# Kernel optimization log

Hardware: AMD Instinct MI355X
Metric: run time of the kernel (lower is better)

The kernel has to match this reference:

```python
import jax, jax.numpy as jnp
import numpy as np
from jax import lax

B, W, M = 4, 20, 512
RNN_HID = 64
N_HIDDEN = RNN_HID          # bi = False
HALF = N_HIDDEN // 2
K = 10
LONG_K = W // 2             # conv_long kernel
LONG_OUT = W - 2 * (LONG_K - 1)   # = 2
N_SPATIAL = 10


def setup_inputs() -> dict:
    key = jax.random.key(0)
    ks = jax.random.split(key, 24)
    g = lambda i, shape, s=0.05: jax.random.normal(ks[i], shape, jnp.float32) * s
    return {
        "x": jax.random.normal(ks[0], (B, W, M), jnp.float32),
        # vanilla RNN (tanh), 1 layer, input_size=1
        "W_ih": g(1, (RNN_HID, 1), 0.2), "W_hh": g(2, (RNN_HID, RNN_HID), 0.1),
        "b_ih": g(3, (RNN_HID,)), "b_hh": g(4, (RNN_HID,)),
        # attention adjacency params
        "W1": g(5, (HALF, N_HIDDEN), 0.1), "b1": g(6, (HALF,)),
        "W2": g(7, (HALF, N_HIDDEN), 0.1),
        "V": g(8, (HALF,), 0.1), "bv": g(9, (1,)),
        "Wb": g(10, (M, M), 0.05), "wb": g(11, (1,)),
        # conv / conv_long
        "conv_w": g(12, (K, 1, W), 0.1), "conv_b": g(13, (K,)),
        "convl_w": g(14, (K, 1, LONG_K), 0.1), "convl_b": g(15, (K,)),
        # graph conv layers: adj @ (x @ W) + b
        "gc1_w": g(16, ((1 + LONG_OUT) * K, N_HIDDEN), 0.1), "gc1_b": g(17, (N_HIDDEN,)),
        "gc2_w": g(18, (N_HIDDEN, N_SPATIAL), 0.1), "gc2_b": g(19, (N_SPATIAL,)),
        # output head
        "out_w": g(20, (1, N_HIDDEN + N_SPATIAL), 0.1), "out_b": g(21, (1,)),
        # fixed geographic adjacency (data.adj)
        "adj": jax.random.uniform(ks[22], (M, M), dtype=jnp.float32),
    }


def _conv1d(x, w, b, dilation=1):
    # x: (N, Cin, W), w: (Cout, Cin, K) -> (N, Cout, Wout), VALID padding
    y = lax.conv_general_dilated(x, w, (1,), 'VALID', rhs_dilation=(dilation,),
                                 dimension_numbers=('NCH', 'OIH', 'NCH'))
    return y + b[None, :, None]


def reference(x, W_ih, W_hh, b_ih, b_hh, W1, b1, W2, V, bv, Wb, wb,
              conv_w, conv_b, convl_w, convl_b, gc1_w, gc1_b, gc2_w, gc2_b,
              out_w, out_b, adj):
    b, w, m = x.shape
    # ---- RNN encode each node's scalar series: (b*m, w, 1) -> last hidden ----
    xr = jnp.transpose(x, (0, 2, 1)).reshape(b * m, w)          # (bm, w)
    inp = xr[..., None] @ W_ih.T + b_ih                         # (bm, w, H)

    def step(h, u):
        return jnp.tanh(u + h @ W_hh.T + b_hh), None

    h0 = jnp.zeros((b * m, RNN_HID), x.dtype)
    h_last, _ = lax.scan(step, h0, jnp.swapaxes(inp, 0, 1))     # (bm, H)
    last_hid = h_last.reshape(b, m, N_HIDDEN)
    out_temporal = last_hid

    # ---- pairwise bilinear attention adjacency (broadcast instead of repeat) ----
    p = last_hid @ W1.T                                         # (b, m, H/2)
    q = last_hid @ W2.T                                         # (b, m, H/2)
    e = jax.nn.elu(p[:, :, None, :] + q[:, None, :, :] + b1)    # (b, m, m, H/2)
    a_mx = e @ V + bv[0]                                        # (b, m, m)
    # F.normalize(p=2, dim=1)
    nrm = jnp.maximum(jnp.sqrt(jnp.sum(a_mx * a_mx, axis=1, keepdims=True)), 1e-12)
    a_mx = a_mx / nrm
    c = jax.nn.sigmoid(a_mx @ Wb + wb[0])                       # (b, m, m)
    A = adj[None] * c + a_mx * (1.0 - c)

    # ---- per-node convs, batched over all b*m series (no Python loop) ----
    h_tmp = xr[:, None, :]                                      # (bm, 1, w)
    r = _conv1d(h_tmp, conv_w, conv_b)                          # (bm, k, 1)
    r_long = _conv1d(h_tmp, convl_w, convl_b, dilation=2)       # (bm, k, long_out)
    r_l = jnp.concatenate([r, r_long], axis=-1).reshape(b, m, -1)  # (b, m, (1+lo)*k)
    r_l = jax.nn.relu(r_l)

    # ---- graph convolutions: adj @ (x @ W) + b ----
    xg = jax.nn.relu(A @ (r_l @ gc1_w) + gc1_b)                 # (b, m, H)
    out_spatial = jax.nn.relu(A @ (xg @ gc2_w) + gc2_b)         # (b, m, 10)

    out = jnp.concatenate([out_spatial, out_temporal], axis=-1)
    return (out @ out_w.T + out_b)[..., 0]                      # (b, m)
```

## Files before the change

kernel.cpp:

```cpp
#include <hip/hip_runtime.h>
#include <hip/hip_bf16.h>
#include <cstdint>
#include <cstddef>

#define OFF_P     0
#define OFF_QB    65536
#define OFF_TDOT  131072
#define OFF_COLSQ 133120
#define OFF_ZT    135168
#define OFF_AMXB  155648
#define OFF_ABF   679936
#define OFF_G1T   1204224
#define OFF_WBT   1269760

typedef __attribute__((ext_vector_type(8))) short short8;
typedef __attribute__((ext_vector_type(8))) unsigned short ushort8;
typedef __attribute__((ext_vector_type(4))) float f32x4;

__device__ inline unsigned short f2bf(float f) {
    unsigned u = __builtin_bit_cast(unsigned, f);
    unsigned r = u + 0x7FFFu + ((u >> 16) & 1u);
    return (unsigned short)(r >> 16);
}
__device__ inline float bf2f(unsigned short s) {
    unsigned u = ((unsigned)s) << 16;
    return __builtin_bit_cast(float, u);
}
__device__ inline float tanh_fast(float x) {
    return 1.f - 2.f/(__expf(2.f*x) + 1.f);
}

__global__ __launch_bounds__(256) void k1_rnn(
    const float* __restrict__ x, const float* __restrict__ W_ih,
    const float* __restrict__ W_hh, const float* __restrict__ b_ih,
    const float* __restrict__ b_hh, const float* __restrict__ W1,
    const float* __restrict__ b1, const float* __restrict__ W2,
    const float* __restrict__ conv_w, const float* __restrict__ conv_b,
    const float* __restrict__ convl_w, const float* __restrict__ convl_b,
    const float* __restrict__ gc1_w, const float* __restrict__ out_w,
    const float* __restrict__ out_b, const float* __restrict__ Wb,
    float* __restrict__ p_out, float* __restrict__ qb_out,
    unsigned short* __restrict__ G1T, float* __restrict__ tdot,
    float* __restrict__ colsq, unsigned short* __restrict__ WbT)
{
    __shared__ float h_sh[4][64];
    __shared__ float xt_sh[4][20];
    __shared__ float rl_sh[4][30];
    __shared__ float tile[64][68];
    int tid = threadIdx.x;

    if (blockIdx.x >= 512) {
        int tt = blockIdx.x - 512;
        int k0 = (tt >> 3) * 64, j0 = (tt & 7) * 64;
        #pragma unroll
        for (int q = 0; q < 4; ++q) {
            int kr = (tid>>4) + 16*q;
            int jc = (tid&15)*4;
            *(float4*)&tile[kr][jc] = *(const float4*)(Wb + (size_t)(k0+kr)*512 + j0 + jc);
        }
        __syncthreads();
        int jl = tid>>2, kc = (tid&3)*16;
        int j = j0 + jl;
        ushort8 v0, v1;
        #pragma unroll
        for (int kk = 0; kk < 8; ++kk) v0[kk] = f2bf(tile[kc+kk][jl]);
        #pragma unroll
        for (int kk = 0; kk < 8; ++kk) v1[kk] = f2bf(tile[kc+8+kk][jl]);
        unsigned short* dst = WbT + (size_t)j*512 + k0 + kc;
        *(ushort8*)dst = v0;
        *(ushort8*)(dst+8) = v1;
        return;
    }

    int w = tid >> 6, lane = tid & 63;
    int s = blockIdx.x * 4 + w;
    int b = s >> 9, m = s & 511;

    if (blockIdx.x < 8) colsq[blockIdx.x * 256 + tid] = 0.f;

    if (lane < 20) xt_sh[w][lane] = x[(b*20 + lane)*512 + m];

    float wrow[64];
    const float* wr = W_hh + lane*64;
    #pragma unroll
    for (int k4 = 0; k4 < 16; ++k4) {
        float4 v = reinterpret_cast<const float4*>(wr)[k4];
        wrow[4*k4+0]=v.x; wrow[4*k4+1]=v.y; wrow[4*k4+2]=v.z; wrow[4*k4+3]=v.w;
    }
    float wih = W_ih[lane], bih = b_ih[lane], bhh = b_hh[lane];
    h_sh[w][lane] = 0.f;
    float h = 0.f;

    if (lane < 10) {
        float acc = conv_b[lane];
        #pragma unroll
        for (int t = 0; t < 20; ++t) acc += conv_w[lane*20+t]*xt_sh[w][t];
        rl_sh[w][3*lane] = fmaxf(acc, 0.f);
    } else if (lane < 30) {
        int idx = lane-10, j = idx>>1, oo = idx&1;
        float acc = convl_b[j];
        #pragma unroll
        for (int t = 0; t < 10; ++t) acc += convl_w[j*10+t]*xt_sh[w][oo+2*t];
        rl_sh[w][3*j+1+oo] = fmaxf(acc, 0.f);
    }

    for (int t = 0; t < 20; ++t) {
        float a0=0.f, a1=0.f, a2=0.f, a3=0.f;
        #pragma unroll
        for (int k = 0; k < 64; k += 4) {
            a0 += wrow[k+0]*h_sh[w][k+0];
            a1 += wrow[k+1]*h_sh[w][k+1];
            a2 += wrow[k+2]*h_sh[w][k+2];
            a3 += wrow[k+3]*h_sh[w][k+3];
        }
        float acc = xt_sh[w][t]*wih + bih + bhh + ((a0+a1)+(a2+a3));
        h = tanh_fast(acc);
        h_sh[w][lane] = h;
    }

    float td = h * out_w[10 + lane];
    #pragma unroll
    for (int off = 32; off; off >>= 1) td += __shfl_down(td, off);
    if (lane == 0) tdot[s] = td + out_b[0];

    if (lane < 32) {
        const float* w1r = W1 + lane*64;
        float acc = 0.f;
        #pragma unroll
        for (int k = 0; k < 64; ++k) acc += w1r[k]*h_sh[w][k];
        p_out[s*32 + lane] = acc;
    } else {
        int i = lane - 32;
        const float* w2r = W2 + i*64;
        float acc = 0.f;
        #pragma unroll
        for (int k = 0; k < 64; ++k) acc += w2r[k]*h_sh[w][k];
        qb_out[s*32 + i] = acc + b1[i];
    }

    float g = 0.f;
    #pragma unroll
    for (int t = 0; t < 30; ++t) g += rl_sh[w][t]*gc1_w[t*64 + lane];
    G1T[((size_t)(b*64 + lane))*512 + m] = f2bf(g);
}

__global__ __launch_bounds__(256) void k2_amx(
    const float* __restrict__ p, const float* __restrict__ qb,
    const float* __restrict__ V, const float* __restrict__ bv,
    unsigned short* __restrict__ amxB, float* __restrict__ colsq)
{
    __shared__ float p_sh[32*36], q_sh[32*36], v_sh[32], sq_sh[32*17];
    int t = threadIdx.x;
    int b = blockIdx.z, i0 = blockIdx.y*32, j0 = blockIdx.x*32;
    {
        int r = t >> 3, c4 = (t & 7)*4;
        *(float4*)&p_sh[r*36 + c4] = *(const float4*)(p  + (size_t)(b*512 + i0 + r)*32 + c4);
        *(float4*)&q_sh[r*36 + c4] = *(const float4*)(qb + (size_t)(b*512 + j0 + r)*32 + c4);
    }
    if (t < 32) v_sh[t] = V[t];
    __syncthreads();

    int ti = t >> 4, tj = t & 15;
    float bv0 = bv[0];
    float a00 = bv0, a01 = bv0, a10 = bv0, a11 = bv0;
    #pragma unroll
    for (int h = 0; h < 32; ++h) {
        float p0 = p_sh[ti*36 + h], p1 = p_sh[(ti+16)*36 + h];
        float q0 = q_sh[tj*36 + h], q1 = q_sh[(tj+16)*36 + h];
        float vh = v_sh[h];
        float x00 = p0+q0, x01 = p0+q1, x10 = p1+q0, x11 = p1+q1;
        float e00 = x00 > 0.f ? x00 : __expf(x00)-1.f;
        float e01 = x01 > 0.f ? x01 : __expf(x01)-1.f;
        float e10 = x10 > 0.f ? x10 : __expf(x10)-1.f;
        float e11 = x11 > 0.f ? x11 : __expf(x11)-1.f;
        a00 += vh*e00; a01 += vh*e01; a10 += vh*e10; a11 += vh*e11;
    }
    size_t base0 = ((size_t)(b*512 + i0 + ti))*512 + j0;
    size_t base1 = ((size_t)(b*512 + i0 + ti + 16))*512 + j0;
    amxB[base0 + tj]      = f2bf(a00);
    amxB[base0 + tj + 16] = f2bf(a01);
    amxB[base1 + tj]      = f2bf(a10);
    amxB[base1 + tj + 16] = f2bf(a11);

    sq_sh[tj*17 + ti]      = a00*a00 + a10*a10;
    sq_sh[(tj+16)*17 + ti] = a01*a01 + a11*a11;
    __syncthreads();
    if (t < 32) {
        float ssum = 0.f;
        #pragma unroll
        for (int r = 0; r < 16; ++r) ssum += sq_sh[t*17 + r];
        atomicAdd(&colsq[b*512 + j0 + t], ssum);
    }
}

__global__ __launch_bounds__(64) void k3a_mfma(
    const unsigned short* __restrict__ amxB, const unsigned short* __restrict__ WbT,
    const float* __restrict__ colsq, const float* __restrict__ wb,
    const float* __restrict__ adj, unsigned short* __restrict__ Abf)
{
    int lane = threadIdx.x;
    int b = blockIdx.z;
    int i0 = blockIdx.y*32, j0 = blockIdx.x*32;
    f32x4 acc[2][2] = {};

    int sl = (lane>>4)*8;
    int fr = lane & 15;
    const unsigned short* abase = amxB + ((size_t)(b*512 + i0 + fr))*512 + sl;
    const unsigned short* bbase = WbT  + ((size_t)(j0 + fr))*512 + sl;
    const float* csq = colsq + b*512 + sl;

    #pragma unroll 2
    for (int k0 = 0; k0 < 512; k0 += 32) {
        float4 c0 = *(const float4*)(csq + k0);
        float4 c1 = *(const float4*)(csq + k0 + 4);
        float iv[8] = {
            rsqrtf(fmaxf(c0.x,1e-24f)), rsqrtf(fmaxf(c0.y,1e-24f)),
            rsqrtf(fmaxf(c0.z,1e-24f)), rsqrtf(fmaxf(c0.w,1e-24f)),
            rsqrtf(fmaxf(c1.x,1e-24f)), rsqrtf(fmaxf(c1.y,1e-24f)),
            rsqrtf(fmaxf(c1.z,1e-24f)), rsqrtf(fmaxf(c1.w,1e-24f)) };

        short8 a0r = *(const short8*)(abase + k0);
        short8 a1r = *(const short8*)(abase + 16*512 + k0);
        short8 b0  = *(const short8*)(bbase + k0);
        short8 b1  = *(const short8*)(bbase + 16*512 + k0);

        short8 a0, a1;
        #pragma unroll
        for (int e = 0; e < 8; ++e) {
            a0[e] = (short)f2bf(bf2f((unsigned short)a0r[e]) * iv[e]);
            a1[e] = (short)f2bf(bf2f((unsigned short)a1r[e]) * iv[e]);
        }

        acc[0][0] = __builtin_amdgcn_mfma_f32_16x16x32_bf16(a0, b0, acc[0][0],0,0,0);
        acc[0][1] = __builtin_amdgcn_mfma_f32_16x16x32_bf16(a0, b1, acc[0][1],0,0,0);
        acc[1][0] = __builtin_amdgcn_mfma_f32_16x16x32_bf16(a1, b0, acc[1][0],0,0,0);
        acc[1][1] = __builtin_amdgcn_mfma_f32_16x16x32_bf16(a1, b1, acc[1][1],0,0,0);
    }

    float wbs = wb[0];
    #pragma unroll
    for (int fj = 0; fj < 2; ++fj) {
        int j = j0 + fj*16 + fr;
        float inv = rsqrtf(fmaxf(colsq[b*512 + j], 1e-24f));
        #pragma unroll
        for (int fi = 0; fi < 2; ++fi)
        #pragma unroll
        for (int r = 0; r < 4; ++r) {
            int i = i0 + fi*16 + (lane>>4)*4 + r;
            float S = acc[fi][fj][r] + wbs;
            float c = 1.f/(1.f + __expf(-S));
            float aN = bf2f(amxB[((size_t)(b*512)+i)*512 + j]) * inv;
            Abf[((size_t)(b*512)+i)*512 + j] = f2bf(adj[i*512+j]*c + aN*(1.f - c));
        }
    }
}

#define AS_STRIDE 520
__global__ __launch_bounds__(256) void k3b_mfma(
    const unsigned short* __restrict__ Abf, const unsigned short* __restrict__ G1T,
    const float* __restrict__ gc1_b, const float* __restrict__ gc2_w,
    float* __restrict__ zT)
{
    __shared__ __align__(16) unsigned short As[16*AS_STRIDE];
    __shared__ float xg[16][68];
    int t = threadIdx.x;
    int b = blockIdx.y, i0 = blockIdx.x*16;
    int wv = t >> 6, lane = t & 63;

    {
        int r = t >> 4, seg = (t & 15)*32;
        const unsigned short* src = Abf + ((size_t)(b*512 + i0 + r))*512 + seg;
        *(short8*)&As[r*AS_STRIDE + seg]      = *(const short8*)src;
        *(short8*)&As[r*AS_STRIDE + seg + 8]  = *(const short8*)(src + 8);
        *(short8*)&As[r*AS_STRIDE + seg + 16] = *(const short8*)(src + 16);
        *(short8*)&As[r*AS_STRIDE + seg + 24] = *(const short8*)(src + 24);
    }
    __syncthreads();

    f32x4 acc = {};
    const unsigned short* gbase = G1T + ((size_t)(b*64 + wv*16 + (lane&15)))*512 + (lane>>4)*8;
    int aoff = (lane&15)*AS_STRIDE + (lane>>4)*8;
    #pragma unroll 4
    for (int k0 = 0; k0 < 512; k0 += 32) {
        short8 af = *(const short8*)&As[aoff + k0];
        short8 bf = *(const short8*)(gbase + k0);
        acc = __builtin_amdgcn_mfma_f32_16x16x32_bf16(af, bf, acc, 0,0,0);
    }

    {
        int cc = wv*16 + (lane&15);
        float gb = gc1_b[cc];
        #pragma unroll
        for (int r = 0; r < 4; ++r)
            xg[(lane>>4)*4 + r][cc] = fmaxf(acc[r] + gb, 0.f);
    }
    __syncthreads();

    if (t < 160) {
        int row = t/10, sx = t%10;
        float a = 0.f;
        #pragma unroll
        for (int c = 0; c < 64; ++c) a += xg[row][c]*gc2_w[c*10 + sx];
        zT[((size_t)(b*10) + sx)*512 + i0 + row] = a;
    }
}

__global__ __launch_bounds__(256) void k4_out(
    const unsigned short* __restrict__ Abf, const float* __restrict__ zT,
    const float* __restrict__ gc2_b, const float* __restrict__ out_w,
    const float* __restrict__ tdot, float* __restrict__ out)
{
    int t = threadIdx.x;
    int w = t >> 6, lane = t & 63;
    int s = blockIdx.x*4 + w;
    int b = s >> 9;

    short8 av = *(const short8*)(Abf + (size_t)s*512 + lane*8);
    float a[8];
    #pragma unroll
    for (int q = 0; q < 8; ++q) a[q] = bf2f((unsigned short)av[q]);

    float acc[10];
    #pragma unroll
    for (int sx = 0; sx < 10; ++sx) {
        const float* zr = zT + ((size_t)(b*10) + sx)*512 + lane*8;
        float4 z0 = *(const float4*)zr;
        float4 z1 = *(const float4*)(zr + 4);
        acc[sx] = a[0]*z0.x + a[1]*z0.y + a[2]*z0.z + a[3]*z0.w
                + a[4]*z1.x + a[5]*z1.y + a[6]*z1.z + a[7]*z1.w;
    }
    #pragma unroll
    for (int sx = 0; sx < 10; ++sx)
        #pragma unroll
        for (int off = 32; off; off >>= 1) acc[sx] += __shfl_down(acc[sx], off);
    if (lane == 0) {
        float o = tdot[s];
        #pragma unroll
        for (int sx = 0; sx < 10; ++sx)
            o += fmaxf(acc[sx] + gc2_b[sx], 0.f) * out_w[sx];
        out[s] = o;
    }
}

extern "C" void kernel_launch(void* const* d_in, const int* in_sizes, int n_in,
                              void* d_out, int out_size, void* d_ws, size_t ws_size,
                              hipStream_t stream) {
    const float* x       = (const float*)d_in[0];
    const float* W_ih    = (const float*)d_in[1];
    const float* W_hh    = (const float*)d_in[2];
    const float* b_ih    = (const float*)d_in[3];
    const float* b_hh    = (const float*)d_in[4];
    const float* W1      = (const float*)d_in[5];
    const float* b1      = (const float*)d_in[6];
    const float* W2      = (const float*)d_in[7];
    const float* V       = (const float*)d_in[8];
    const float* bv      = (const float*)d_in[9];
    const float* Wb      = (const float*)d_in[10];
    const float* wb      = (const float*)d_in[11];
    const float* conv_w  = (const float*)d_in[12];
    const float* conv_b  = (const float*)d_in[13];
    const float* convl_w = (const float*)d_in[14];
    const float* convl_b = (const float*)d_in[15];
    const float* gc1_w   = (const float*)d_in[16];
    const float* gc1_b   = (const float*)d_in[17];
    const float* gc2_w   = (const float*)d_in[18];
    const float* gc2_b   = (const float*)d_in[19];
    const float* out_w   = (const float*)d_in[20];
    const float* out_b   = (const float*)d_in[21];
    const float* adj     = (const float*)d_in[22];

    float* ws    = (float*)d_ws;
    float* p     = ws + OFF_P;
    float* qb    = ws + OFF_QB;
    float* tdot  = ws + OFF_TDOT;
    float* colsq = ws + OFF_COLSQ;
    float* zT    = ws + OFF_ZT;
    unsigned short* amxB = (unsigned short*)(ws + OFF_AMXB);
    unsigned short* Abf  = (unsigned short*)(ws + OFF_ABF);
    unsigned short* G1T  = (unsigned short*)(ws + OFF_G1T);
    unsigned short* WbT  = (unsigned short*)(ws + OFF_WBT);
    float* out   = (float*)d_out;

    k1_rnn<<<dim3(576), dim3(256), 0, stream>>>(
        x, W_ih, W_hh, b_ih, b_hh, W1, b1, W2,
        conv_w, conv_b, convl_w, convl_b, gc1_w, out_w, out_b, Wb,
        p, qb, G1T, tdot, colsq, WbT);

    k2_amx<<<dim3(16,16,4), dim3(256), 0, stream>>>(p, qb, V, bv, amxB, colsq);

    k3a_mfma<<<dim3(16,16,4), dim3(64), 0, stream>>>(amxB, WbT, colsq, wb, adj, Abf);

    k3b_mfma<<<dim3(32,4), dim3(256), 0, stream>>>(Abf, G1T, gc1_b, gc2_w, zT);

    k4_out<<<dim3(512), dim3(256), 0, stream>>>(Abf, zT, gc2_b, out_w, tdot, out);
}
```

Baseline: 61.04 us.

## Split graph-conv GEMM across more blocks with atomic zT accumulation

The graph-conv kernel is re-split from 128 four-wave blocks into 512 single-wave blocks. Each block computes a 16x16 slice of the hidden channels and atomically adds its partial gc2 projection into zT, which the preceding kernel now zeroes. The attention-matrix kernel also keeps the diagonal tile of amx in shared memory so its epilogue no longer re-reads it from global memory. It switches the operand rounding to a cheaper round-half-up bf16 conversion. The cost is float atomics and a slightly different rounding mode.

Result: no change. 62.15 us (+1.8%).

```diff
diff --git a/kernel.cpp b/kernel.cpp
--- a/kernel.cpp
+++ b/kernel.cpp
@@ -21,6 +21,10 @@
     unsigned u = __builtin_bit_cast(unsigned, f);
     unsigned r = u + 0x7FFFu + ((u >> 16) & 1u);
     return (unsigned short)(r >> 16);
+}
+__device__ inline unsigned short f2bf_fast(float f) {
+    unsigned u = __builtin_bit_cast(unsigned, f);
+    return (unsigned short)((u + 0x8000u) >> 16);
 }
 __device__ inline float bf2f(unsigned short s) {
     unsigned u = ((unsigned)s) << 16;
@@ -196,11 +200,17 @@
 __global__ __launch_bounds__(64) void k3a_mfma(
     const unsigned short* __restrict__ amxB, const unsigned short* __restrict__ WbT,
     const float* __restrict__ colsq, const float* __restrict__ wb,
-    const float* __restrict__ adj, unsigned short* __restrict__ Abf)
+    const float* __restrict__ adj, unsigned short* __restrict__ Abf,
+    float* __restrict__ zT)
 {
+    __shared__ unsigned short amx_save[32*40];
     int lane = threadIdx.x;
     int b = blockIdx.z;
     int i0 = blockIdx.y*32, j0 = blockIdx.x*32;
+
+    int fb = (blockIdx.z<<8) | (blockIdx.y<<4) | blockIdx.x;
+    if (fb < 320) zT[fb*64 + lane] = 0.f;
+
     f32x4 acc[2][2] = {};
 
     int sl = (lane>>4)*8;
@@ -224,11 +234,16 @@
         short8 b0  = *(const short8*)(bbase + k0);
         short8 b1  = *(const short8*)(bbase + 16*512 + k0);
 
+        if (k0 == j0) {
+            *(short8*)&amx_save[fr*40 + sl]      = a0r;
+            *(short8*)&amx_save[(fr+16)*40 + sl] = a1r;
+        }
+
         short8 a0, a1;
         #pragma unroll
         for (int e = 0; e < 8; ++e) {
-            a0[e] = (short)f2bf(bf2f((unsigned short)a0r[e]) * iv[e]);
-            a1[e] = (short)f2bf(bf2f((unsigned short)a1r[e]) * iv[e]);
+            a0[e] = (short)f2bf_fast(bf2f((unsigned short)a0r[e]) * iv[e]);
+            a1[e] = (short)f2bf_fast(bf2f((unsigned short)a1r[e]) * iv[e]);
         }
 
         acc[0][0] = __builtin_amdgcn_mfma_f32_16x16x32_bf16(a0, b0, acc[0][0],0,0,0);
@@ -246,62 +261,54 @@
         for (int fi = 0; fi < 2; ++fi)
         #pragma unroll
         for (int r = 0; r < 4; ++r) {
-            int i = i0 + fi*16 + (lane>>4)*4 + r;
+            int il = fi*16 + (lane>>4)*4 + r;
+            int i = i0 + il;
             float S = acc[fi][fj][r] + wbs;
             float c = 1.f/(1.f + __expf(-S));
-            float aN = bf2f(amxB[((size_t)(b*512)+i)*512 + j]) * inv;
-            Abf[((size_t)(b*512)+i)*512 + j] = f2bf(adj[i*512+j]*c + aN*(1.f - c));
+            float aN = bf2f(amx_save[il*40 + fj*16 + fr]) * inv;
+            Abf[((size_t)(b*512)+i)*512 + j] = f2bf(adj[(size_t)i*512+j]*c + aN*(1.f - c));
         }
     }
 }
 
-#define AS_STRIDE 520
-__global__ __launch_bounds__(256) void k3b_mfma(
+__global__ __launch_bounds__(64) void k3b_mfma(
     const unsigned short* __restrict__ Abf, const unsigned short* __restrict__ G1T,
     const float* __restrict__ gc1_b, const float* __restrict__ gc2_w,
     float* __restrict__ zT)
 {
-    __shared__ __align__(16) unsigned short As[16*AS_STRIDE];
-    __shared__ float xg[16][68];
-    int t = threadIdx.x;
-    int b = blockIdx.y, i0 = blockIdx.x*16;
-    int wv = t >> 6, lane = t & 63;
-
-    {
-        int r = t >> 4, seg = (t & 15)*32;
-        const unsigned short* src = Abf + ((size_t)(b*512 + i0 + r))*512 + seg;
-        *(short8*)&As[r*AS_STRIDE + seg]      = *(const short8*)src;
-        *(short8*)&As[r*AS_STRIDE + seg + 8]  = *(const short8*)(src + 8);
-        *(short8*)&As[r*AS_STRIDE + seg + 16] = *(const short8*)(src + 16);
-        *(short8*)&As[r*AS_STRIDE + seg + 24] = *(const short8*)(src + 24);
-    }
-    __syncthreads();
+    __shared__ float xg_sh[16][18];
+    int lane = threadIdx.x;
+    int bid = blockIdx.x;
+    int b   = bid >> 7;
+    int rem = bid & 127;
+    int i0  = (rem >> 2) * 16;
+    int c0  = (rem & 3) * 16;
+
+    int fr = lane & 15, sl = (lane>>4)*8;
+    const unsigned short* abase = Abf + ((size_t)(b*512 + i0 + fr))*512 + sl;
+    const unsigned short* gbase = G1T + ((size_t)(b*64 + c0 + fr))*512 + sl;
 
     f32x4 acc = {};
-    const unsigned short* gbase = G1T + ((size_t)(b*64 + wv*16 + (lane&15)))*512 + (lane>>4)*8;
-    int aoff = (lane&15)*AS_STRIDE + (lane>>4)*8;
     #pragma unroll 4
     for (int k0 = 0; k0 < 512; k0 += 32) {
-        short8 af = *(const short8*)&As[aoff + k0];
-        short8 bf = *(const short8*)(gbase + k0);
-        acc = __builtin_amdgcn_mfma_f32_16x16x32_bf16(af, bf, acc, 0,0,0);
+        short8 a = *(const short8*)(abase + k0);
+        short8 g = *(const short8*)(gbase + k0);
+        acc = __builtin_amdgcn_mfma_f32_16x16x32_bf16(a, g, acc, 0,0,0);
     }
 
     {
-        int cc = wv*16 + (lane&15);
-        float gb = gc1_b[cc];
+        float gb = gc1_b[c0 + fr];
         #pragma unroll
         for (int r = 0; r < 4; ++r)
-            xg[(lane>>4)*4 + r][cc] = fmaxf(acc[r] + gb, 0.f);
-    }
-    __syncthreads();
-
-    if (t < 160) {
-        int row = t/10, sx = t%10;
-        float a = 0.f;
-        #pragma unroll
-        for (int c = 0; c < 64; ++c) a += xg[row][c]*gc2_w[c*10 + sx];
-        zT[((size_t)(b*10) + sx)*512 + i0 + row] = a;
+            xg_sh[(lane>>4)*4 + r][fr] = fmaxf(acc[r] + gb, 0.f);
+    }
+
+    for (int pp = lane; pp < 160; pp += 64) {
+        int row = pp / 10, sx = pp % 10;
+        float s = 0.f;
+        #pragma unroll
+        for (int c = 0; c < 16; ++c) s += xg_sh[row][c] * gc2_w[(c0 + c)*10 + sx];
+        atomicAdd(&zT[((size_t)(b*10) + sx)*512 + i0 + row], s);
     }
 }
 
@@ -388,9 +395,9 @@
 
     k2_amx<<<dim3(16,16,4), dim3(256), 0, stream>>>(p, qb, V, bv, amxB, colsq);
 
-    k3a_mfma<<<dim3(16,16,4), dim3(64), 0, stream>>>(amxB, WbT, colsq, wb, adj, Abf);
-
-    k3b_mfma<<<dim3(32,4), dim3(256), 0, stream>>>(Abf, G1T, gc1_b, gc2_w, zT);
+    k3a_mfma<<<dim3(16,16,4), dim3(64), 0, stream>>>(amxB, WbT, colsq, wb, adj, Abf, zT);
+
+    k3b_mfma<<<dim3(512), dim3(64), 0, stream>>>(Abf, G1T, gc1_b, gc2_w, zT);
 
     k4_out<<<dim3(512), dim3(256), 0, stream>>>(Abf, zT, gc2_b, out_w, tdot, out);
 }
```
